# Optimization experiments

Measured on AMD Instinct MI355X. Metric: run time of the kernel, lower is better.

The kernel has to match this reference:

```python
import jax, jax.numpy as jnp
import numpy as np

B, S, HID = 1, 2048, 2048
H, HKV, D = 16, 4, 128
GROUPS = H // HKV
SCALE = D ** -0.5


def rotate_half(x):
    x1, x2 = x[..., : x.shape[-1] // 2], x[..., x.shape[-1] // 2 :]
    return jnp.concatenate((-x2, x1), axis=-1)


def setup_inputs() -> dict:
    key = jax.random.key(0)
    ks = jax.random.split(key, 8)
    hidden_states = jax.random.normal(ks[0], (B, S, HID), dtype=jnp.float32)
    # standard RoPE tables, base 10000
    inv_freq = 1.0 / (10000.0 ** (np.arange(0, D, 2, dtype=np.float32) / D))
    t = np.arange(S, dtype=np.float32)
    freqs = np.outer(t, inv_freq)                      # (S, D/2)
    emb = np.concatenate([freqs, freqs], axis=-1)      # (S, D)
    cos = jnp.asarray(np.cos(emb)[None], dtype=jnp.float32)  # (1, S, D)
    sin = jnp.asarray(np.sin(emb)[None], dtype=jnp.float32)
    std = 0.02
    Wq = jax.random.normal(ks[1], (HID, H * D), dtype=jnp.float32) * std
    Wk = jax.random.normal(ks[2], (HID, HKV * D), dtype=jnp.float32) * std
    Wv = jax.random.normal(ks[3], (HID, HKV * D), dtype=jnp.float32) * std
    Wg = jax.random.normal(ks[4], (HID, HKV), dtype=jnp.float32) * std
    Wo = jax.random.normal(ks[5], (H * D, HID), dtype=jnp.float32) * std
    return {"hidden_states": hidden_states, "cos": cos, "sin": sin,
            "Wq": Wq, "Wk": Wk, "Wv": Wv, "Wg": Wg, "Wo": Wo}


def reference(hidden_states, cos, sin, Wq, Wk, Wv, Wg, Wo):
    b, s, _ = hidden_states.shape
    # projections -> (B, heads, S, D)
    q = (hidden_states @ Wq).reshape(b, s, H, D).transpose(0, 2, 1, 3)
    k = (hidden_states @ Wk).reshape(b, s, HKV, D).transpose(0, 2, 1, 3)
    v = (hidden_states @ Wv).reshape(b, s, HKV, D).transpose(0, 2, 1, 3)
    g = (hidden_states @ Wg).transpose(0, 2, 1)                 # (B, HKV, S)
    g = jax.nn.log_sigmoid(g.astype(jnp.float32))
    # RoPE
    c, sn = cos[:, None, :, :], sin[:, None, :, :]
    q = q * c + rotate_half(q) * sn
    k = k * c + rotate_half(k) * sn
    # GQA repeat kv heads
    k = jnp.repeat(k, GROUPS, axis=1)
    v = jnp.repeat(v, GROUPS, axis=1)
    g = jnp.repeat(g, GROUPS, axis=1)                           # (B, H, S)
    # gated power retention, deg=2, parallel (quadratic) form
    G = jnp.cumsum(g, axis=-1)                                  # (B, H, S)
    # decay_ij = exp(G_i - G_j) for j <= i  (<= 1 since logsigmoid < 0)
    logdecay = G[..., :, None] - G[..., None, :]                # (B, H, S, S)
    causal = jnp.tril(jnp.ones((s, s), dtype=bool))
    decay = jnp.where(causal, jnp.exp(logdecay), 0.0)
    qk = jnp.einsum("bhid,bhjd->bhij", q, k) * SCALE
    scores = (qk * qk) * decay                                  # deg=2 power scores
    den = jnp.maximum(jnp.sum(scores, axis=-1, keepdims=True), 1.0)
    out = jnp.einsum("bhij,bhjd->bhid", scores, v) / den        # (B, H, S, D)
    out = out.transpose(0, 2, 1, 3).reshape(b, s, H * D)
    return out @ Wo
```

## Files before the change

kernel.cpp:

```cpp
#include <hip/hip_runtime.h>
#include <hip/hip_bf16.h>

#define S_LEN 2048
#define HID   2048
#define NH    16
#define NKV   4
#define HD    128
#define KVD   512
#define NQKV  3072
#define SCALE2 0.0078125f
#define NCH   80

typedef __bf16 bf16;
typedef __attribute__((ext_vector_type(8))) __bf16 bf16x8;
typedef __attribute__((ext_vector_type(4))) float f32x4;

__device__ __forceinline__ void gload_lds16(const bf16* g, bf16* l) {
    __builtin_amdgcn_global_load_lds((const __attribute__((address_space(1))) void*)g,
                                     (__attribute__((address_space(3))) void*)l, 16, 0, 0);
}

__device__ __forceinline__ void transpose_tile(const float* __restrict__ W,
                                               bf16* __restrict__ Wt,
                                               int K, int N, int bx, int by,
                                               int t, float (*Ts)[65])
{
    const int kb = bx * 64, nb = by * 64;
    const int tr = t >> 6, tc = t & 63;
    #pragma unroll
    for (int p = 0; p < 16; ++p) {
        int k = p * 4 + tr;
        Ts[k][tc] = W[(size_t)(kb + k) * N + nb + tc];
    }
    __syncthreads();
    const int nr = t >> 3, kc = t & 7;
    #pragma unroll
    for (int p = 0; p < 2; ++p) {
        int n = p * 32 + nr;
        bf16x8 o;
        #pragma unroll
        for (int x = 0; x < 8; ++x) o[x] = (bf16)Ts[kc * 8 + x][n];
        *(bf16x8*)&Wt[(size_t)(nb + n) * K + kb + kc * 8] = o;
    }
}

__global__ __launch_bounds__(256) void prep_kernel(const float* __restrict__ hs,
                                                   const float* __restrict__ Wq,
                                                   const float* __restrict__ Wk,
                                                   const float* __restrict__ Wv,
                                                   const float* __restrict__ Wo,
                                                   const float* __restrict__ Wg,
                                                   bf16* __restrict__ hsb,
                                                   bf16* __restrict__ WcatT,
                                                   bf16* __restrict__ WoT,
                                                   float* __restrict__ graw,
                                                   float* __restrict__ outz)
{
    __shared__ float Ts[64][65];
    const int b = blockIdx.x, tid = threadIdx.x;

    if (b < 2048) {
        int i = (b * 256 + tid) * 8;
        const float4* qp = (const float4*)&hs[i];
        float4 a = qp[0], c = qp[1];
        bf16x8 r;
        r[0]=(bf16)a.x; r[1]=(bf16)a.y; r[2]=(bf16)a.z; r[3]=(bf16)a.w;
        r[4]=(bf16)c.x; r[5]=(bf16)c.y; r[6]=(bf16)c.z; r[7]=(bf16)c.w;
        *(bf16x8*)&hsb[i] = r;
    } else if (b < 3072) {
        int lb = b - 2048;
        transpose_tile(Wq, WcatT, HID, HID, lb >> 5, lb & 31, tid, Ts);
    } else if (b < 3328) {
        int lb = b - 3072;
        transpose_tile(Wk, WcatT + (size_t)2048 * HID, HID, KVD, lb >> 3, lb & 7, tid, Ts);
    } else if (b < 3584) {
        int lb = b - 3328;
        transpose_tile(Wv, WcatT + (size_t)2560 * HID, HID, KVD, lb >> 3, lb & 7, tid, Ts);
    } else if (b < 4608) {
        int lb = b - 3584;
        transpose_tile(Wo, WoT, HID, HID, lb >> 5, lb & 31, tid, Ts);
    } else if (b < 6656) {
        int i = ((b - 4608) * 256 + tid) * 8;
        float4 z = make_float4(0.f, 0.f, 0.f, 0.f);
        *(float4*)&outz[i] = z;
        *(float4*)&outz[i + 4] = z;
    } else {
        const int w = tid >> 6, lane = tid & 63;
        const int s = (b - 6656) * 4 + w;
        float a0 = 0.f, a1 = 0.f, a2 = 0.f, a3 = 0.f;
        for (int kk = lane; kk < HID; kk += 64) {
            float h = hs[(size_t)s * HID + kk];
            const float* wr = &Wg[kk * 4];
            a0 += h * wr[0]; a1 += h * wr[1];
            a2 += h * wr[2]; a3 += h * wr[3];
        }
        #pragma unroll
        for (int off = 32; off >= 1; off >>= 1) {
            a0 += __shfl_xor(a0, off); a1 += __shfl_xor(a1, off);
            a2 += __shfl_xor(a2, off); a3 += __shfl_xor(a3, off);
        }
        if (lane == 0) {
            float vv[4] = {a0, a1, a2, a3};
            #pragma unroll
            for (int c = 0; c < 4; ++c) {
                float x = vv[c];
                graw[c * S_LEN + s] = fminf(x, 0.f) - log1pf(expf(-fabsf(x)));
            }
        }
    }
}

__global__ __launch_bounds__(256) void cumsum_kernel(const float* __restrict__ graw,
                                                     float* __restrict__ G)
{
    int c = blockIdx.x, t = threadIdx.x;
    __shared__ float sums[256];
    float loc[8];
    float run = 0.f;
    #pragma unroll
    for (int i = 0; i < 8; ++i) { run += graw[c * S_LEN + t * 8 + i]; loc[i] = run; }
    sums[t] = run;
    __syncthreads();
    for (int off = 1; off < 256; off <<= 1) {
        float add = (t >= off) ? sums[t - off] : 0.f;
        __syncthreads();
        sums[t] += add;
        __syncthreads();
    }
    float offset = sums[t] - run;
    #pragma unroll
    for (int i = 0; i < 8; ++i) G[c * S_LEN + t * 8 + i] = offset + loc[i];
}

__device__ __forceinline__ void gemm128_core(const bf16* __restrict__ A,
                                             const bf16* __restrict__ Bt,
                                             int K, int k0, int k1, int mb, int nb,
                                             bf16 (*As)[32], bf16 (*Bs)[32],
                                             f32x4 (*acc)[4],
                                             int w, int l16, int quad, int lane)
{
    const int m0 = (w & 1) * 64, n0 = (w >> 1) * 64;
    const int srow = lane >> 2, scol = (lane & 3) * 8;

    for (int kt = k0; kt < k1; kt += 32) {
        __syncthreads();
        gload_lds16(&A [(size_t)(mb + w * 32 +      srow) * K + kt + scol], &As[w * 32     ][0]);
        gload_lds16(&A [(size_t)(mb + w * 32 + 16 + srow) * K + kt + scol], &As[w * 32 + 16][0]);
        gload_lds16(&Bt[(size_t)(nb + w * 32 +      srow) * K + kt + scol], &Bs[w * 32     ][0]);
        gload_lds16(&Bt[(size_t)(nb + w * 32 + 16 + srow) * K + kt + scol], &Bs[w * 32 + 16][0]);
        __syncthreads();

        bf16x8 af[4], bfr[4];
        #pragma unroll
        for (int t = 0; t < 4; ++t) af[t]  = *(const bf16x8*)&As[m0 + t * 16 + l16][quad * 8];
        #pragma unroll
        for (int u = 0; u < 4; ++u) bfr[u] = *(const bf16x8*)&Bs[n0 + u * 16 + l16][quad * 8];
        #pragma unroll
        for (int t = 0; t < 4; ++t)
            #pragma unroll
            for (int u = 0; u < 4; ++u)
                acc[t][u] = __builtin_amdgcn_mfma_f32_16x16x32_bf16(af[t], bfr[u], acc[t][u], 0, 0, 0);
    }
}

__global__ __launch_bounds__(256) void gemm_qkv_kernel(const bf16* __restrict__ A,
                                                       const bf16* __restrict__ Wt,
                                                       bf16* __restrict__ qOut,
                                                       bf16* __restrict__ kOut,
                                                       bf16* __restrict__ vOut,
                                                       int M, int K)
{
    __shared__ __attribute__((aligned(16))) bf16 As[128][32];
    __shared__ __attribute__((aligned(16))) bf16 Bs[128][32];
    const int tid = threadIdx.x, w = tid >> 6, lane = tid & 63;
    const int l16 = lane & 15, quad = lane >> 4;
    const int mb = blockIdx.x * 128, nb = blockIdx.y * 128;
    const int m0 = (w & 1) * 64, n0 = (w >> 1) * 64;

    f32x4 acc[4][4] = {};
    gemm128_core(A, Wt, K, 0, K, mb, nb, As, Bs, acc, w, l16, quad, lane);

    #pragma unroll
    for (int t = 0; t < 4; ++t)
        #pragma unroll
        for (int u = 0; u < 4; ++u)
            #pragma unroll
            for (int r = 0; r < 4; ++r) {
                int row = mb + m0 + t * 16 + quad * 4 + r;
                int col = nb + n0 + u * 16 + l16;
                bf16 val = (bf16)acc[t][u][r];
                if (nb < 2048)       qOut[(size_t)row * HID + col] = val;
                else if (nb < 2560)  kOut[(size_t)row * KVD + (col - 2048)] = val;
                else                 vOut[(size_t)(col - 2560) * S_LEN + row] = val;
            }
}

__global__ __launch_bounds__(256) void gemm_wo_kernel(const bf16* __restrict__ A,
                                                      const bf16* __restrict__ Bt,
                                                      float* __restrict__ C,
                                                      int M, int N, int K)
{
    __shared__ __attribute__((aligned(16))) bf16 As[128][32];
    __shared__ __attribute__((aligned(16))) bf16 Bs[128][32];
    const int tid = threadIdx.x, w = tid >> 6, lane = tid & 63;
    const int l16 = lane & 15, quad = lane >> 4;
    const int mb = blockIdx.x * 128, nb = blockIdx.y * 128;
    const int m0 = (w & 1) * 64, n0 = (w >> 1) * 64;
    const int kh = K >> 1, k0 = blockIdx.z * kh;

    f32x4 acc[4][4] = {};
    gemm128_core(A, Bt, K, k0, k0 + kh, mb, nb, As, Bs, acc, w, l16, quad, lane);

    #pragma unroll
    for (int t = 0; t < 4; ++t)
        #pragma unroll
        for (int u = 0; u < 4; ++u)
            #pragma unroll
            for (int r = 0; r < 4; ++r) {
                int row = mb + m0 + t * 16 + quad * 4 + r;
                int col = nb + n0 + u * 16 + l16;
                unsafeAtomicAdd(&C[(size_t)row * N + col], acc[t][u][r]);
            }
}

__global__ __launch_bounds__(256) void rope_kernel(bf16* __restrict__ qb,
                                                   bf16* __restrict__ kb,
                                                   const float* __restrict__ cosb,
                                                   const float* __restrict__ sinb)
{
    int idx = blockIdx.x * 256 + threadIdx.x;
    bf16* x; int s, rem, stride;
    if (idx < S_LEN * NH * 64) {
        x = qb; stride = HID;
        s = idx / (NH * 64); rem = idx % (NH * 64);
    } else {
        idx -= S_LEN * NH * 64;
        x = kb; stride = KVD;
        s = idx / (NKV * 64); rem = idx % (NKV * 64);
    }
    int h = rem >> 6, d = rem & 63;
    size_t base = (size_t)s * stride + h * 128 + d;
    float x0 = (float)x[base], x1 = (float)x[base + 64];
    float c0 = cosb[s * 128 + d], c1 = cosb[s * 128 + d + 64];
    float n0 = sinb[s * 128 + d], n1 = sinb[s * 128 + d + 64];
    x[base]      = (bf16)(x0 * c0 - x1 * n0);
    x[base + 64] = (bf16)(x1 * c1 + x0 * n1);
}

__global__ __launch_bounds__(256) void attn_kernel(const bf16* __restrict__ q,
                                                   const bf16* __restrict__ k,
                                                   const bf16* __restrict__ vT,
                                                   const float* __restrict__ G,
                                                   bf16* __restrict__ out,
                                                   float* __restrict__ pO,
                                                   float* __restrict__ pden)
{
    int rem = blockIdx.x, qt = 0, cch = 0;
    #pragma unroll
    for (int g = 0; g < 4; ++g) {
        int sz = 8 * (g + 1);
        if (rem < sz) { qt = g * 8 + rem / (g + 1); cch = rem % (g + 1); break; }
        rem -= sz;
    }
    const int gg = qt >> 3, nc = gg + 1;
    const int jt0 = cch * 8, jt1 = min(qt + 1, jt0 + 8);

    const int h = blockIdx.y, kvh = h >> 2;
    const int qb = qt * 64;
    const int tid = threadIdx.x, w = tid >> 6, lane = tid & 63;
    const int l16 = lane & 15, quad = lane >> 4;

    __shared__ __attribute__((aligned(16))) bf16 Ks4[4][64][32];
    __shared__ __attribute__((aligned(16))) bf16 Vt4[2][128][32];
    __shared__ __attribute__((aligned(16))) bf16 Sb[4][16][68];

    bf16x8 qf[4];
    const int qrow = qb + w * 16 + l16;
    #pragma unroll
    for (int kc = 0; kc < 4; ++kc)
        qf[kc] = *(const bf16x8*)&q[(size_t)qrow * HID + h * HD + kc * 32 + quad * 8];

    const int irow = qb + w * 16 + quad * 4;
    float Gq[4];
    #pragma unroll
    for (int r = 0; r < 4; ++r) Gq[r] = G[kvh * S_LEN + irow + r];

    const int sr4 = lane >> 2, sc4 = (lane & 3) * 8;
    const int vkk = w >> 1, vdg = (w & 1) * 4;

    f32x4 acco[8] = {};
    float den[4] = {0.f, 0.f, 0.f, 0.f};

    for (int kt = jt0; kt < jt1; ++kt) {
        const int jb = kt * 64;
        __syncthreads();
        #pragma unroll
        for (int rg = 0; rg < 4; ++rg)
            gload_lds16(&k[(size_t)(jb + rg * 16 + sr4) * KVD + kvh * HD + w * 32 + sc4],
                        &Ks4[w][rg * 16][0]);
        #pragma unroll
        for (int it = 0; it < 4; ++it)
            gload_lds16(&vT[(size_t)(kvh * HD + (vdg + it) * 16 + sr4) * S_LEN + jb + vkk * 32 + sc4],
                        &Vt4[vkk][(vdg + it) * 16][0]);
        __syncthreads();

        f32x4 accs[4] = {};
        #pragma unroll
        for (int t = 0; t < 4; ++t)
            #pragma unroll
            for (int kc = 0; kc < 4; ++kc) {
                bf16x8 bfr = *(const bf16x8*)&Ks4[kc][t * 16 + l16][quad * 8];
                accs[t] = __builtin_amdgcn_mfma_f32_16x16x32_bf16(qf[kc], bfr, accs[t], 0, 0, 0);
            }

        const float Gt = G[kvh * S_LEN + jb];
        float sr[4];
        #pragma unroll
        for (int r = 0; r < 4; ++r) sr[r] = SCALE2 * __expf(Gq[r] - Gt);
        #pragma unroll
        for (int t = 0; t < 4; ++t) {
            int j = jb + t * 16 + l16;
            float colF = __expf(fminf(Gt - G[kvh * S_LEN + j], 85.f));
            #pragma unroll
            for (int r = 0; r < 4; ++r) {
                float d0 = accs[t][r];
                float sc = (j <= irow + r) ? d0 * d0 * sr[r] * colF : 0.f;
                den[r] += sc;
                Sb[w][quad * 4 + r][t * 16 + l16] = (bf16)sc;
            }
        }

        #pragma unroll
        for (int kk = 0; kk < 2; ++kk) {
            bf16x8 af = *(const bf16x8*)&Sb[w][l16][kk * 32 + quad * 8];
            #pragma unroll
            for (int dt = 0; dt < 8; ++dt) {
                bf16x8 bfr = *(const bf16x8*)&Vt4[kk][dt * 16 + l16][quad * 8];
                acco[dt] = __builtin_amdgcn_mfma_f32_16x16x32_bf16(af, bfr, acco[dt], 0, 0, 0);
            }
        }
    }

    #pragma unroll
    for (int r = 0; r < 4; ++r) {
        #pragma unroll
        for (int off = 1; off < 16; off <<= 1) den[r] += __shfl_xor(den[r], off);
    }

    if (nc == 1) {
        float dinv[4];
        #pragma unroll
        for (int r = 0; r < 4; ++r) dinv[r] = 1.f / fmaxf(den[r], 1.f);
        #pragma unroll
        for (int dt = 0; dt < 8; ++dt)
            #pragma unroll
            for (int r = 0; r < 4; ++r)
                out[(size_t)(irow + r) * HID + h * HD + dt * 16 + l16] =
                    (bf16)(acco[dt][r] * dinv[r]);
    } else {
        const int slot = h * NCH + 4 * gg * (gg + 1) + (qt & 7) * (gg + 1) + cch;
        float* po = &pO[(size_t)slot * 8192];
        const int lr = w * 16 + quad * 4;
        #pragma unroll
        for (int dt = 0; dt < 8; ++dt)
            #pragma unroll
            for (int r = 0; r < 4; ++r)
                po[(lr + r) * 128 + dt * 16 + l16] = acco[dt][r];
        if (l16 == 0) {
            #pragma unroll
            for (int r = 0; r < 4; ++r) pden[slot * 64 + lr + r] = den[r];
        }
    }
}

__global__ __launch_bounds__(256) void attn_reduce_kernel(const float* __restrict__ pO,
                                                          const float* __restrict__ pden,
                                                          bf16* __restrict__ out)
{
    const int p = blockIdx.x;
    const int h = p / 24, qt = 8 + p % 24;
    const int gg = qt >> 3, nc = gg + 1;
    const int base = h * NCH + 4 * gg * (gg + 1) + (qt & 7) * (gg + 1);
    const int qb = qt * 64;
    const int tid = threadIdx.x;

    __shared__ float sden[64];
    if (tid < 64) {
        float s = 0.f;
        for (int c = 0; c < nc; ++c) s += pden[(base + c) * 64 + tid];
        sden[tid] = 1.f / fmaxf(s, 1.f);
    }
    __syncthreads();

    #pragma unroll
    for (int i = 0; i < 8; ++i) {
        int e = i * 1024 + tid * 4;
        float4 s = make_float4(0.f, 0.f, 0.f, 0.f);
        for (int c = 0; c < nc; ++c) {
            float4 v = *(const float4*)&pO[(size_t)(base + c) * 8192 + e];
            s.x += v.x; s.y += v.y; s.z += v.z; s.w += v.w;
        }
        int lr = e >> 7, col = e & 127;
        float di = sden[lr];
        bf16* o = &out[(size_t)(qb + lr) * HID + h * HD + col];
        o[0] = (bf16)(s.x * di); o[1] = (bf16)(s.y * di);
        o[2] = (bf16)(s.z * di); o[3] = (bf16)(s.w * di);
    }
}

extern "C" void kernel_launch(void* const* d_in, const int* in_sizes, int n_in,
                              void* d_out, int out_size, void* d_ws, size_t ws_size,
                              hipStream_t stream)
{
    const float* hs   = (const float*)d_in[0];
    const float* cosb = (const float*)d_in[1];
    const float* sinb = (const float*)d_in[2];
    const float* Wq   = (const float*)d_in[3];
    const float* Wk   = (const float*)d_in[4];
    const float* Wv   = (const float*)d_in[5];
    const float* Wg   = (const float*)d_in[6];
    const float* Wo   = (const float*)d_in[7];
    float* out = (float*)d_out;

    char* p = (char*)d_ws;
    bf16*  qbuf  = (bf16*)p;  p += (size_t)S_LEN * HID * 2;
    bf16*  kbuf  = (bf16*)p;  p += (size_t)S_LEN * KVD * 2;
    bf16*  vT    = (bf16*)p;  p += (size_t)S_LEN * KVD * 2;
    bf16*  abuf  = (bf16*)p;  p += (size_t)S_LEN * HID * 2;
    bf16*  hsb   = (bf16*)p;  p += (size_t)S_LEN * HID * 2;
    bf16*  WcatT = (bf16*)p;  p += (size_t)NQKV * HID * 2;
    bf16*  WoT   = (bf16*)p;  p += (size_t)HID * HID * 2;
    float* graw  = (float*)p; p += (size_t)NKV * S_LEN * 4;
    float* G     = (float*)p; p += (size_t)NKV * S_LEN * 4;
    float* pO    = (float*)p; p += (size_t)NH * NCH * 8192 * 4;
    float* pden  = (float*)p; p += (size_t)NH * NCH * 64 * 4;

    prep_kernel<<<7168, 256, 0, stream>>>(hs, Wq, Wk, Wv, Wo, Wg,
                                          hsb, WcatT, WoT, graw, out);
    cumsum_kernel<<<NKV, 256, 0, stream>>>(graw, G);
    gemm_qkv_kernel<<<dim3(16, 24), 256, 0, stream>>>(hsb, WcatT, qbuf, kbuf, vT, S_LEN, HID);
    rope_kernel<<<(S_LEN * NH * 64 + S_LEN * NKV * 64) / 256, 256, 0, stream>>>(qbuf, kbuf, cosb, sinb);
    attn_kernel<<<dim3(NCH, NH), 256, 0, stream>>>(qbuf, kbuf, vT, G, abuf, pO, pden);
    attn_reduce_kernel<<<NH * 24, 256, 0, stream>>>(pO, pden, abuf);
    gemm_wo_kernel<<<dim3(16, 16, 2), 256, 0, stream>>>(abuf, WoT, out, S_LEN, HID, HID);
}
```

Baseline: 300.5 us.

## Split-K the QKV GEMM into fp32 scratch and raise Wo split-K to four

The QKV projection GEMM now splits K in two across blockIdx.z and accumulates with fp32 atomics into zeroed scratch buffers that reuse the pO workspace. The RoPE kernel reads these fp32 buffers, applies rotation, and writes bf16 q/k; it also converts V to bf16. The Wo GEMM split-K factor rises from 2 to 4. The aim is more blocks in flight for the small 384-block grids, at the cost of extra zeroing, atomic traffic and fp32 intermediate bandwidth.

```diff
diff --git a/kernel.cpp b/kernel.cpp
--- a/kernel.cpp
+++ b/kernel.cpp
@@ -54,7 +54,8 @@
                                                    bf16* __restrict__ WcatT,
                                                    bf16* __restrict__ WoT,
                                                    float* __restrict__ graw,
-                                                   float* __restrict__ outz)
+                                                   float* __restrict__ outz,
+                                                   float* __restrict__ qkvf)
 {
     __shared__ float Ts[64][65];
     const int b = blockIdx.x, tid = threadIdx.x;
@@ -84,7 +85,7 @@
         float4 z = make_float4(0.f, 0.f, 0.f, 0.f);
         *(float4*)&outz[i] = z;
         *(float4*)&outz[i + 4] = z;
-    } else {
+    } else if (b < 7168) {
         const int w = tid >> 6, lane = tid & 63;
         const int s = (b - 6656) * 4 + w;
         float a0 = 0.f, a1 = 0.f, a2 = 0.f, a3 = 0.f;
@@ -107,6 +108,11 @@
                 graw[c * S_LEN + s] = fminf(x, 0.f) - log1pf(expf(-fabsf(x)));
             }
         }
+    } else {
+        int i = ((b - 7168) * 256 + tid) * 8;
+        float4 z = make_float4(0.f, 0.f, 0.f, 0.f);
+        *(float4*)&qkvf[i] = z;
+        *(float4*)&qkvf[i + 4] = z;
     }
 }
 
@@ -165,40 +171,10 @@
 
 __global__ __launch_bounds__(256) void gemm_qkv_kernel(const bf16* __restrict__ A,
                                                        const bf16* __restrict__ Wt,
-                                                       bf16* __restrict__ qOut,
-                                                       bf16* __restrict__ kOut,
-                                                       bf16* __restrict__ vOut,
+                                                       float* __restrict__ qf,
+                                                       float* __restrict__ kf,
+                                                       float* __restrict__ vf,
                                                        int M, int K)
-{
-    __shared__ __attribute__((aligned(16))) bf16 As[128][32];
-    __shared__ __attribute__((aligned(16))) bf16 Bs[128][32];
-    const int tid = threadIdx.x, w = tid >> 6, lane = tid & 63;
-    const int l16 = lane & 15, quad = lane >> 4;
-    const int mb = blockIdx.x * 128, nb = blockIdx.y * 128;
-    const int m0 = (w & 1) * 64, n0 = (w >> 1) * 64;
-
-    f32x4 acc[4][4] = {};
-    gemm128_core(A, Wt, K, 0, K, mb, nb, As, Bs, acc, w, l16, quad, lane);
-
-    #pragma unroll
-    for (int t = 0; t < 4; ++t)
-        #pragma unroll
-        for (int u = 0; u < 4; ++u)
-            #pragma unroll
-            for (int r = 0; r < 4; ++r) {
-                int row = mb + m0 + t * 16 + quad * 4 + r;
-                int col = nb + n0 + u * 16 + l16;
-                bf16 val = (bf16)acc[t][u][r];
-                if (nb < 2048)       qOut[(size_t)row * HID + col] = val;
-                else if (nb < 2560)  kOut[(size_t)row * KVD + (col - 2048)] = val;
-                else                 vOut[(size_t)(col - 2560) * S_LEN + row] = val;
-            }
-}
-
-__global__ __launch_bounds__(256) void gemm_wo_kernel(const bf16* __restrict__ A,
-                                                      const bf16* __restrict__ Bt,
-                                                      float* __restrict__ C,
-                                                      int M, int N, int K)
 {
     __shared__ __attribute__((aligned(16))) bf16 As[128][32];
     __shared__ __attribute__((aligned(16))) bf16 Bs[128][32];
@@ -209,6 +185,37 @@
     const int kh = K >> 1, k0 = blockIdx.z * kh;
 
     f32x4 acc[4][4] = {};
+    gemm128_core(A, Wt, K, k0, k0 + kh, mb, nb, As, Bs, acc, w, l16, quad, lane);
+
+    #pragma unroll
+    for (int t = 0; t < 4; ++t)
+        #pragma unroll
+        for (int u = 0; u < 4; ++u)
+            #pragma unroll
+            for (int r = 0; r < 4; ++r) {
+                int row = mb + m0 + t * 16 + quad * 4 + r;
+                int col = nb + n0 + u * 16 + l16;
+                float val = acc[t][u][r];
+                if (nb < 2048)       unsafeAtomicAdd(&qf[(size_t)row * HID + col], val);
+                else if (nb < 2560)  unsafeAtomicAdd(&kf[(size_t)row * KVD + (col - 2048)], val);
+                else                 unsafeAtomicAdd(&vf[(size_t)(col - 2560) * S_LEN + row], val);
+            }
+}
+
+__global__ __launch_bounds__(256) void gemm_wo_kernel(const bf16* __restrict__ A,
+                                                      const bf16* __restrict__ Bt,
+                                                      float* __restrict__ C,
+                                                      int M, int N, int K)
+{
+    __shared__ __attribute__((aligned(16))) bf16 As[128][32];
+    __shared__ __attribute__((aligned(16))) bf16 Bs[128][32];
+    const int tid = threadIdx.x, w = tid >> 6, lane = tid & 63;
+    const int l16 = lane & 15, quad = lane >> 4;
+    const int mb = blockIdx.x * 128, nb = blockIdx.y * 128;
+    const int m0 = (w & 1) * 64, n0 = (w >> 1) * 64;
+    const int kh = K >> 2, k0 = blockIdx.z * kh;
+
+    f32x4 acc[4][4] = {};
     gemm128_core(A, Bt, K, k0, k0 + kh, mb, nb, As, Bs, acc, w, l16, quad, lane);
 
     #pragma unroll
@@ -223,28 +230,45 @@
             }
 }
 
-__global__ __launch_bounds__(256) void rope_kernel(bf16* __restrict__ qb,
+#define RQ_N (S_LEN * NH * 64)
+#define RK_N (S_LEN * NKV * 64)
+#define RV_N (S_LEN * KVD / 8)
+__global__ __launch_bounds__(256) void rope_kernel(const float* __restrict__ qf,
+                                                   const float* __restrict__ kf,
+                                                   const float* __restrict__ vf,
+                                                   bf16* __restrict__ qb,
                                                    bf16* __restrict__ kb,
+                                                   bf16* __restrict__ vT,
                                                    const float* __restrict__ cosb,
                                                    const float* __restrict__ sinb)
 {
     int idx = blockIdx.x * 256 + threadIdx.x;
-    bf16* x; int s, rem, stride;
-    if (idx < S_LEN * NH * 64) {
-        x = qb; stride = HID;
-        s = idx / (NH * 64); rem = idx % (NH * 64);
+    if (idx < RQ_N + RK_N) {
+        const float* src; bf16* dst; int s, rem, stride;
+        if (idx < RQ_N) {
+            src = qf; dst = qb; stride = HID;
+            s = idx / (NH * 64); rem = idx % (NH * 64);
+        } else {
+            idx -= RQ_N;
+            src = kf; dst = kb; stride = KVD;
+            s = idx / (NKV * 64); rem = idx % (NKV * 64);
+        }
+        int h = rem >> 6, d = rem & 63;
+        size_t base = (size_t)s * stride + h * 128 + d;
+        float x0 = src[base], x1 = src[base + 64];
+        float c0 = cosb[s * 128 + d], c1 = cosb[s * 128 + d + 64];
+        float n0 = sinb[s * 128 + d], n1 = sinb[s * 128 + d + 64];
+        dst[base]      = (bf16)(x0 * c0 - x1 * n0);
+        dst[base + 64] = (bf16)(x1 * c1 + x0 * n1);
     } else {
-        idx -= S_LEN * NH * 64;
-        x = kb; stride = KVD;
-        s = idx / (NKV * 64); rem = idx % (NKV * 64);
-    }
-    int h = rem >> 6, d = rem & 63;
-    size_t base = (size_t)s * stride + h * 128 + d;
-    float x0 = (float)x[base], x1 = (float)x[base + 64];
-    float c0 = cosb[s * 128 + d], c1 = cosb[s * 128 + d + 64];
-    float n0 = sinb[s * 128 + d], n1 = sinb[s * 128 + d + 64];
-    x[base]      = (bf16)(x0 * c0 - x1 * n0);
-    x[base + 64] = (bf16)(x1 * c1 + x0 * n1);
+        int i = (idx - RQ_N - RK_N) * 8;
+        const float4* qp = (const float4*)&vf[i];
+        float4 a = qp[0], c = qp[1];
+        bf16x8 r;
+        r[0]=(bf16)a.x; r[1]=(bf16)a.y; r[2]=(bf16)a.z; r[3]=(bf16)a.w;
+        r[4]=(bf16)c.x; r[5]=(bf16)c.y; r[6]=(bf16)c.z; r[7]=(bf16)c.w;
+        *(bf16x8*)&vT[i] = r;
+    }
 }
 
 __global__ __launch_bounds__(256) void attn_kernel(const bf16* __restrict__ q,
@@ -435,12 +459,16 @@
     float* pO    = (float*)p; p += (size_t)NH * NCH * 8192 * 4;
     float* pden  = (float*)p; p += (size_t)NH * NCH * 64 * 4;
 
-    prep_kernel<<<7168, 256, 0, stream>>>(hs, Wq, Wk, Wv, Wo, Wg,
-                                          hsb, WcatT, WoT, graw, out);
+    float* qf = pO;
+    float* kf = pO + (size_t)4 * 1024 * 1024;
+    float* vf = pO + (size_t)5 * 1024 * 1024;
+
+    prep_kernel<<<10240, 256, 0, stream>>>(hs, Wq, Wk, Wv, Wo, Wg,
+                                           hsb, WcatT, WoT, graw, out, qf);
     cumsum_kernel<<<NKV, 256, 0, stream>>>(graw, G);
-    gemm_qkv_kernel<<<dim3(16, 24), 256, 0, stream>>>(hsb, WcatT, qbuf, kbuf, vT, S_LEN, HID);
-    rope_kernel<<<(S_LEN * NH * 64 + S_LEN * NKV * 64) / 256, 256, 0, stream>>>(qbuf, kbuf, cosb, sinb);
+    gemm_qkv_kernel<<<dim3(16, 24, 2), 256, 0, stream>>>(hsb, WcatT, qf, kf, vf, S_LEN, HID);
+    rope_kernel<<<(RQ_N + RK_N + RV_N) / 256, 256, 0, stream>>>(qf, kf, vf, qbuf, kbuf, vT, cosb, sinb);
     attn_kernel<<<dim3(NCH, NH), 256, 0, stream>>>(qbuf, kbuf, vT, G, abuf, pO, pden);
     attn_reduce_kernel<<<NH * 24, 256, 0, stream>>>(pO, pden, abuf);
-    gemm_wo_kernel<<<dim3(16, 16, 2), 256, 0, stream>>>(abuf, WoT, out, S_LEN, HID, HID);
-}
+    gemm_wo_kernel<<<dim3(16, 16, 4), 256, 0, stream>>>(abuf, WoT, out, S_LEN, HID, HID);
+}
```

Result: slower. 348.9 us (+16.1%).

## Split-K the QKV GEMM into fp32 slices and fold cumsum into RoPE kernel

Applied to the files above, without the earlier changes.

The QKV projection GEMM gets a 2-way split over K (grid z=2), so 768 blocks run instead of 384 and the GPU's compute units are better occupied. Each half writes fp32 partials into scratch space reused from the pO and abuf buffers. The RoPE kernel then sums the two partials, applies RoPE, converts to bf16, and also reduces the V slices; the separate cumsum kernel is merged into it as extra blocks to save a launch. The cost is extra fp32 write and read traffic for the partials, and reusing those buffers depends on their lifetimes not overlapping.

```diff
diff --git a/kernel.cpp b/kernel.cpp
--- a/kernel.cpp
+++ b/kernel.cpp
@@ -110,28 +110,6 @@
     }
 }
 
-__global__ __launch_bounds__(256) void cumsum_kernel(const float* __restrict__ graw,
-                                                     float* __restrict__ G)
-{
-    int c = blockIdx.x, t = threadIdx.x;
-    __shared__ float sums[256];
-    float loc[8];
-    float run = 0.f;
-    #pragma unroll
-    for (int i = 0; i < 8; ++i) { run += graw[c * S_LEN + t * 8 + i]; loc[i] = run; }
-    sums[t] = run;
-    __syncthreads();
-    for (int off = 1; off < 256; off <<= 1) {
-        float add = (t >= off) ? sums[t - off] : 0.f;
-        __syncthreads();
-        sums[t] += add;
-        __syncthreads();
-    }
-    float offset = sums[t] - run;
-    #pragma unroll
-    for (int i = 0; i < 8; ++i) G[c * S_LEN + t * 8 + i] = offset + loc[i];
-}
-
 __device__ __forceinline__ void gemm128_core(const bf16* __restrict__ A,
                                              const bf16* __restrict__ Bt,
                                              int K, int k0, int k1, int mb, int nb,
@@ -165,9 +143,9 @@
 
 __global__ __launch_bounds__(256) void gemm_qkv_kernel(const bf16* __restrict__ A,
                                                        const bf16* __restrict__ Wt,
-                                                       bf16* __restrict__ qOut,
-                                                       bf16* __restrict__ kOut,
-                                                       bf16* __restrict__ vOut,
+                                                       float* __restrict__ qsl,
+                                                       float* __restrict__ ksl,
+                                                       float* __restrict__ vsl,
                                                        int M, int K)
 {
     __shared__ __attribute__((aligned(16))) bf16 As[128][32];
@@ -176,9 +154,14 @@
     const int l16 = lane & 15, quad = lane >> 4;
     const int mb = blockIdx.x * 128, nb = blockIdx.y * 128;
     const int m0 = (w & 1) * 64, n0 = (w >> 1) * 64;
+    const int z = blockIdx.z, kh = K >> 1, k0 = z * kh;
+
+    float* qd = qsl + (size_t)z * S_LEN * HID;
+    float* kd = ksl + (size_t)z * S_LEN * KVD;
+    float* vd = vsl + (size_t)z * S_LEN * KVD;
 
     f32x4 acc[4][4] = {};
-    gemm128_core(A, Wt, K, 0, K, mb, nb, As, Bs, acc, w, l16, quad, lane);
+    gemm128_core(A, Wt, K, k0, k0 + kh, mb, nb, As, Bs, acc, w, l16, quad, lane);
 
     #pragma unroll
     for (int t = 0; t < 4; ++t)
@@ -188,10 +171,10 @@
             for (int r = 0; r < 4; ++r) {
                 int row = mb + m0 + t * 16 + quad * 4 + r;
                 int col = nb + n0 + u * 16 + l16;
-                bf16 val = (bf16)acc[t][u][r];
-                if (nb < 2048)       qOut[(size_t)row * HID + col] = val;
-                else if (nb < 2560)  kOut[(size_t)row * KVD + (col - 2048)] = val;
-                else                 vOut[(size_t)(col - 2560) * S_LEN + row] = val;
+                float val = acc[t][u][r];
+                if (nb < 2048)       qd[(size_t)row * HID + col] = val;
+                else if (nb < 2560)  kd[(size_t)row * KVD + (col - 2048)] = val;
+                else                 vd[(size_t)(col - 2560) * S_LEN + row] = val;
             }
 }
 
@@ -223,28 +206,67 @@
             }
 }
 
-__global__ __launch_bounds__(256) void rope_kernel(bf16* __restrict__ qb,
+#define RQB (S_LEN * NH * 64 / 256)
+#define RKB (S_LEN * NKV * 64 / 256)
+#define RVB (S_LEN * KVD / 8 / 256)
+__global__ __launch_bounds__(256) void rope_kernel(const float* __restrict__ qsl,
+                                                   const float* __restrict__ ksl,
+                                                   const float* __restrict__ vsl,
+                                                   bf16* __restrict__ qb,
                                                    bf16* __restrict__ kb,
+                                                   bf16* __restrict__ vT,
                                                    const float* __restrict__ cosb,
-                                                   const float* __restrict__ sinb)
-{
-    int idx = blockIdx.x * 256 + threadIdx.x;
-    bf16* x; int s, rem, stride;
-    if (idx < S_LEN * NH * 64) {
-        x = qb; stride = HID;
-        s = idx / (NH * 64); rem = idx % (NH * 64);
+                                                   const float* __restrict__ sinb,
+                                                   const float* __restrict__ graw,
+                                                   float* __restrict__ G)
+{
+    const int blk = blockIdx.x;
+    if (blk < RQB + RKB) {
+        int idx = blk * 256 + threadIdx.x;
+        const float* src; size_t ssz; bf16* dst; int s, rem, stride;
+        if (blk < RQB) {
+            src = qsl; ssz = (size_t)S_LEN * HID; dst = qb; stride = HID;
+            s = idx / (NH * 64); rem = idx % (NH * 64);
+        } else {
+            idx -= RQB * 256;
+            src = ksl; ssz = (size_t)S_LEN * KVD; dst = kb; stride = KVD;
+            s = idx / (NKV * 64); rem = idx % (NKV * 64);
+        }
+        int h = rem >> 6, d = rem & 63;
+        size_t base = (size_t)s * stride + h * 128 + d;
+        float x0 = src[base]      + src[ssz + base];
+        float x1 = src[base + 64] + src[ssz + base + 64];
+        float c0 = cosb[s * 128 + d], c1 = cosb[s * 128 + d + 64];
+        float n0 = sinb[s * 128 + d], n1 = sinb[s * 128 + d + 64];
+        dst[base]      = (bf16)(x0 * c0 - x1 * n0);
+        dst[base + 64] = (bf16)(x1 * c1 + x0 * n1);
+    } else if (blk < RQB + RKB + RVB) {
+        int i = ((blk - RQB - RKB) * 256 + threadIdx.x) * 8;
+        const size_t ssz = (size_t)S_LEN * KVD;
+        bf16x8 r;
+        #pragma unroll
+        for (int x = 0; x < 8; ++x) r[x] = (bf16)(vsl[i + x] + vsl[ssz + i + x]);
+        *(bf16x8*)&vT[i] = r;
     } else {
-        idx -= S_LEN * NH * 64;
-        x = kb; stride = KVD;
-        s = idx / (NKV * 64); rem = idx % (NKV * 64);
-    }
-    int h = rem >> 6, d = rem & 63;
-    size_t base = (size_t)s * stride + h * 128 + d;
-    float x0 = (float)x[base], x1 = (float)x[base + 64];
-    float c0 = cosb[s * 128 + d], c1 = cosb[s * 128 + d + 64];
-    float n0 = sinb[s * 128 + d], n1 = sinb[s * 128 + d + 64];
-    x[base]      = (bf16)(x0 * c0 - x1 * n0);
-    x[base + 64] = (bf16)(x1 * c1 + x0 * n1);
+        const int c = blk - (RQB + RKB + RVB);
+        const int t = threadIdx.x;
+        __shared__ float sums[256];
+        float loc[8];
+        float run = 0.f;
+        #pragma unroll
+        for (int i = 0; i < 8; ++i) { run += graw[c * S_LEN + t * 8 + i]; loc[i] = run; }
+        sums[t] = run;
+        __syncthreads();
+        for (int off = 1; off < 256; off <<= 1) {
+            float add = (t >= off) ? sums[t - off] : 0.f;
+            __syncthreads();
+            sums[t] += add;
+            __syncthreads();
+        }
+        float offset = sums[t] - run;
+        #pragma unroll
+        for (int i = 0; i < 8; ++i) G[c * S_LEN + t * 8 + i] = offset + loc[i];
+    }
 }
 
 __global__ __launch_bounds__(256) void attn_kernel(const bf16* __restrict__ q,
@@ -435,11 +457,15 @@
     float* pO    = (float*)p; p += (size_t)NH * NCH * 8192 * 4;
     float* pden  = (float*)p; p += (size_t)NH * NCH * 64 * 4;
 
+    float* qsl = pO;
+    float* ksl = pO + (size_t)8 * 1024 * 1024;
+    float* vsl = (float*)abuf;
+
     prep_kernel<<<7168, 256, 0, stream>>>(hs, Wq, Wk, Wv, Wo, Wg,
                                           hsb, WcatT, WoT, graw, out);
-    cumsum_kernel<<<NKV, 256, 0, stream>>>(graw, G);
-    gemm_qkv_kernel<<<dim3(16, 24), 256, 0, stream>>>(hsb, WcatT, qbuf, kbuf, vT, S_LEN, HID);
-    rope_kernel<<<(S_LEN * NH * 64 + S_LEN * NKV * 64) / 256, 256, 0, stream>>>(qbuf, kbuf, cosb, sinb);
+    gemm_qkv_kernel<<<dim3(16, 24, 2), 256, 0, stream>>>(hsb, WcatT, qsl, ksl, vsl, S_LEN, HID);
+    rope_kernel<<<RQB + RKB + RVB + NKV, 256, 0, stream>>>(qsl, ksl, vsl, qbuf, kbuf, vT,
+                                                           cosb, sinb, graw, G);
     attn_kernel<<<dim3(NCH, NH), 256, 0, stream>>>(qbuf, kbuf, vT, G, abuf, pO, pden);
     attn_reduce_kernel<<<NH * 24, 256, 0, stream>>>(pO, pden, abuf);
     gemm_wo_kernel<<<dim3(16, 16, 2), 256, 0, stream>>>(abuf, WoT, out, S_LEN, HID, HID);
```

Result: no change. 296.3 us (-1.4%).
